# Kernel tuning notes

Hardware: AMD Instinct MI355X
Metric: run time of the kernel (lower is better)

## Reference

```python
import jax, jax.numpy as jnp
import numpy as np

B, C, H, W = 4, 512, 48, 48
BN_EPS = 1e-5


def setup_inputs() -> dict:
    key = jax.random.key(0)
    ks = jax.random.split(key, 12)
    s = 1.0 / np.sqrt(C)  # conv2d default init scale for 1x1 kernels
    return {
        "x": jax.random.normal(ks[0], (B, C, H, W), dtype=jnp.float32),
        "from_depth_estimation": jax.random.normal(ks[1], (B, C, H, W), dtype=jnp.float32),
        "w_rgb": jax.random.uniform(ks[2], (C, C), jnp.float32, -s, s),
        "b_rgb": jax.random.uniform(ks[3], (C,), jnp.float32, -s, s),
        "w_lhs": jax.random.uniform(ks[4], (C, C), jnp.float32, -s, s),
        "b_lhs": jax.random.uniform(ks[5], (C,), jnp.float32, -s, s),
        "w_rhs": jax.random.uniform(ks[6], (C, C), jnp.float32, -s, s),
        "b_rhs": jax.random.uniform(ks[7], (C,), jnp.float32, -s, s),
        "w_dec": jax.random.uniform(ks[8], (C, C), jnp.float32, -s, s),
        "b_dec": jax.random.uniform(ks[9], (C,), jnp.float32, -s, s),
        "gamma": jnp.ones((C,), jnp.float32),
        "beta": jnp.zeros((C,), jnp.float32),
    }


def _to_tokens(t):
    # (B,C,H,W) -> (B*H*W, C)
    return t.transpose(0, 2, 3, 1).reshape(-1, t.shape[1])


def reference(x, from_depth_estimation, w_rgb, b_rgb, w_lhs, b_lhs, w_rhs, b_rhs,
              w_dec, b_dec, gamma, beta):
    # 1x1 convs == per-token linear layers; weight layout (out, in)
    xt = _to_tokens(x) @ w_rgb.T + b_rgb          # (N, C)
    dt = _to_tokens(from_depth_estimation)
    lhs = dt @ w_lhs.T + b_lhs                     # (N, C)
    rhs = dt @ w_rhs.T + b_rhs                     # (N, C)

    # global, unscaled attention over all B*H*W tokens (batch dims mixed)
    logits = lhs @ rhs.T                           # (N, N)
    weight = jax.nn.softmax(logits, axis=1)
    enhanced = weight @ xt                         # (N, C)

    enhanced = enhanced.reshape(B, H, W, C).transpose(0, 3, 1, 2)  # (B,C,H,W)

    # decoder: 1x1 conv -> BatchNorm2d (batch stats, training mode) -> ReLU
    y = jnp.einsum('bchw,oc->bohw', enhanced, w_dec) + b_dec[None, :, None, None]
    mean = y.mean(axis=(0, 2, 3), keepdims=True)
    var = y.var(axis=(0, 2, 3), keepdims=True)     # biased variance (torch BN fwd)
    y = (y - mean) * jax.lax.rsqrt(var + BN_EPS)
    y = y * gamma[None, :, None, None] + beta[None, :, None, None]
    return jax.nn.relu(y)
```

## Files before the change

kernel.cpp:

```cpp
#include <hip/hip_runtime.h>
#include <math.h>

#define Bd 4
#define Cd 512
#define Hd 48
#define Wd 48
#define HWd (Hd * Wd)
#define Nd (Bd * HWd)
#define BN_EPS 1e-5f

#define QBLK 32
#define KBLK 128
#define NKS 4
#define KSLEN (Nd / NKS)
#define AITERS (KSLEN / KBLK)

typedef _Float16 half8 __attribute__((ext_vector_type(8)));
typedef _Float16 h4 __attribute__((ext_vector_type(4)));
typedef float f32x16 __attribute__((ext_vector_type(16)));

__device__ inline void gload_lds16(const void* g, void* l) {
    __builtin_amdgcn_global_load_lds((const __attribute__((address_space(1))) void*)g,
                                     (__attribute__((address_space(3))) void*)l, 16, 0, 0);
}

__device__ inline size_t wp_idx(int o, int c) {
    return (((size_t)(o >> 5) * 32 + (c >> 4)) * 64 + ((o & 31) + 32 * ((c >> 3) & 1))) * 8 + (c & 7);
}
__device__ inline size_t qp_idx(int q, int c) {
    return (((size_t)(q >> 5) * 64 + (c >> 3)) * 32 + (q & 31)) * 8 + (c & 7);
}
__device__ inline size_t kp_idx(int n, int o) {
    return ((((size_t)(n >> 7) * 4 + ((n >> 5) & 3)) * 32 + (o >> 4)) * 64
            + ((n & 31) + 32 * ((o >> 3) & 1))) * 8 + (o & 7);
}
__device__ inline size_t vp_idx(int n, int o) {
    return ((((size_t)(n >> 7) * 16 + (o >> 5)) * 8 + ((n >> 4) & 7)) * 64
            + ((o & 31) + 32 * ((n >> 3) & 1))) * 8 + (n & 7);
}

__global__ __launch_bounds__(256) void wpack_k(const float* __restrict__ w0,
                                               const float* __restrict__ w1,
                                               const float* __restrict__ w2,
                                               const float* __restrict__ w3,
                                               _Float16* __restrict__ p0,
                                               _Float16* __restrict__ p1,
                                               _Float16* __restrict__ p2,
                                               _Float16* __restrict__ p3) {
    const float* w; _Float16* p;
    switch (blockIdx.y) {
        case 0: w = w0; p = p0; break;
        case 1: w = w1; p = p1; break;
        case 2: w = w2; p = p2; break;
        default: w = w3; p = p3; break;
    }
    int idx = blockIdx.x * 256 + threadIdx.x;
    int o = idx >> 6;
    int cc = (idx & 63) * 8;
    float4 a = *(const float4*)(w + (size_t)o * 512 + cc);
    float4 b = *(const float4*)(w + (size_t)o * 512 + cc + 4);
    half8 v = {(_Float16)a.x, (_Float16)a.y, (_Float16)a.z, (_Float16)a.w,
               (_Float16)b.x, (_Float16)b.y, (_Float16)b.z, (_Float16)b.w};
    *(half8*)(p + wp_idx(o, cc)) = v;
}

template<int INM, int OUTM>
__global__ __launch_bounds__(256, 2) void linproj_k(const void* __restrict__ in,
                                                    const _Float16* __restrict__ Wp,
                                                    const float* __restrict__ bias,
                                                    void* __restrict__ outp) {
    constexpr bool SWAP = (OUTM == 2);
    __shared__ _Float16 Xs[16384];

    const int tid = threadIdx.x;
    const int wave = tid >> 6;
    const int lane = tid & 63;
    const int l31 = lane & 31;
    const int hi32 = lane >> 5;
    const int n0 = blockIdx.x * 32;
    const int by = blockIdx.y;
    const int b = n0 / HWd;
    const int hw0 = n0 % HWd;

    {
        const int t = tid & 31;
        const int c0 = tid >> 5;
        #pragma unroll 8
        for (int k = 0; k < 64; ++k) {
            int c = c0 + 8 * k;
            float val;
            if (INM == 0)
                val = ((const float*)in)[(size_t)(b * Cd + c) * HWd + hw0 + t];
            else
                val = (float)((const _Float16*)in)[(size_t)c * Nd + n0 + t];
            if (!SWAP)
                Xs[(c >> 3) * 256 + t * 8 + (c & 7)] = (_Float16)val;
            else
                Xs[(c >> 4) * 512 + (t + 32 * ((c >> 3) & 1)) * 8 + (c & 7)] = (_Float16)val;
        }
    }
    __syncthreads();

    #pragma unroll
    for (int ot = 0; ot < 2; ++ot) {
        const int otb = by * 256 + ot * 128 + wave * 32;

        half8 wa[32];
        const _Float16* wpb = Wp + ((size_t)(otb >> 5) * 32) * 512;
        #pragma unroll
        for (int f = 0; f < 32; ++f)
            wa[f] = *(const half8*)(wpb + (size_t)f * 512 + lane * 8);

        f32x16 acc;
        #pragma unroll
        for (int r = 0; r < 16; ++r) acc[r] = 0.f;

        __builtin_amdgcn_s_setprio(1);
        #pragma unroll
        for (int f = 0; f < 32; ++f) {
            if (!SWAP) {
                half8 xb = *(const half8*)(Xs + (2 * f + hi32) * 256 + l31 * 8);
                acc = __builtin_amdgcn_mfma_f32_32x32x16_f16(wa[f], xb, acc, 0, 0, 0);
            } else {
                half8 xa = *(const half8*)(Xs + f * 512 + lane * 8);
                acc = __builtin_amdgcn_mfma_f32_32x32x16_f16(xa, wa[f], acc, 0, 0, 0);
            }
        }
        __builtin_amdgcn_s_setprio(0);

        if (OUTM == 0) {
            _Float16* Qp = (_Float16*)outp;
            #pragma unroll
            for (int q8 = 0; q8 < 4; ++q8) {
                int o = otb + 8 * q8 + 4 * hi32;
                float4 bv = *(const float4*)(bias + o);
                h4 v = {(_Float16)(acc[4 * q8 + 0] + bv.x), (_Float16)(acc[4 * q8 + 1] + bv.y),
                        (_Float16)(acc[4 * q8 + 2] + bv.z), (_Float16)(acc[4 * q8 + 3] + bv.w)};
                *(h4*)(Qp + qp_idx(n0 + l31, o)) = v;
            }
        } else if (OUTM == 1) {
            _Float16* Kp = (_Float16*)outp;
            #pragma unroll
            for (int q8 = 0; q8 < 4; ++q8) {
                int o = otb + 8 * q8 + 4 * hi32;
                float4 bv = *(const float4*)(bias + o);
                h4 v = {(_Float16)(acc[4 * q8 + 0] + bv.x), (_Float16)(acc[4 * q8 + 1] + bv.y),
                        (_Float16)(acc[4 * q8 + 2] + bv.z), (_Float16)(acc[4 * q8 + 3] + bv.w)};
                *(h4*)(Kp + kp_idx(n0 + l31, o)) = v;
            }
        } else if (OUTM == 2) {
            _Float16* Vp = (_Float16*)outp;
            int o = otb + l31;
            float bc = bias[o];
            #pragma unroll
            for (int q8 = 0; q8 < 4; ++q8) {
                int n = n0 + 8 * q8 + 4 * hi32;
                h4 v = {(_Float16)(acc[4 * q8 + 0] + bc), (_Float16)(acc[4 * q8 + 1] + bc),
                        (_Float16)(acc[4 * q8 + 2] + bc), (_Float16)(acc[4 * q8 + 3] + bc)};
                *(h4*)(Vp + vp_idx(n, o)) = v;
            }
        } else {
            float* of = (float*)outp;
            #pragma unroll
            for (int r = 0; r < 16; ++r) {
                int o = otb + (r & 3) + 8 * (r >> 2) + 4 * hi32;
                of[(size_t)(b * Cd + o) * HWd + hw0 + l31] = acc[r] + bias[o];
            }
        }
    }
}

__global__ __launch_bounds__(256, 2) void attn_v5_k(
    const _Float16* __restrict__ Qp,
    const _Float16* __restrict__ Kp,
    const _Float16* __restrict__ Vp,
    _Float16* __restrict__ partH,
    float* __restrict__ marr,
    float* __restrict__ larr) {
    __shared__ _Float16 Qs[64 * 256];
    __shared__ _Float16 Pl[2][16 * 256];
    __shared__ float tm_s[4][32], ls_s[4][32];

    const int tid = threadIdx.x;
    const int wave = tid >> 6;
    const int lane = tid & 63;
    const int l31 = lane & 31;
    const int hi32 = lane >> 5;
    const int nqb = Nd / QBLK;
    const int qb = blockIdx.x % nqb;
    const int ks = blockIdx.x / nqb;
    const int q0 = qb * QBLK;
    const int kbt0 = ks * AITERS;

    {
        const _Float16* Qt = Qp + (size_t)(q0 >> 5) * 16384;
        #pragma unroll
        for (int j = 0; j < 8; ++j) {
            int instr = wave * 8 + j;
            gload_lds16(Qt + (size_t)instr * 512 + lane * 8, (char*)Qs + instr * 1024);
        }
    }
    __syncthreads();

    f32x16 o_acc[4];
    #pragma unroll
    for (int c = 0; c < 4; ++c)
        #pragma unroll
        for (int r = 0; r < 16; ++r) o_acc[c][r] = 0.f;
    float m = -INFINITY, l = 0.f;

    for (int it = 0; it < AITERS; ++it) {
        const _Float16* kp = Kp + ((size_t)(kbt0 + it) * 4 + wave) * 32 * 512;
        half8 ka[32];
        #pragma unroll
        for (int f = 0; f < 32; ++f)
            ka[f] = *(const half8*)(kp + (size_t)f * 512 + lane * 8);

        f32x16 s;
        #pragma unroll
        for (int r = 0; r < 16; ++r) s[r] = 0.f;
        __builtin_amdgcn_s_setprio(1);
        #pragma unroll
        for (int f = 0; f < 32; ++f) {
            half8 qb8 = *(const half8*)(Qs + (2 * f + hi32) * 256 + l31 * 8);
            s = __builtin_amdgcn_mfma_f32_32x32x16_f16(ka[f], qb8, s, 0, 0, 0);
        }
        __builtin_amdgcn_s_setprio(0);

        float tmax = s[0];
        #pragma unroll
        for (int r = 1; r < 16; ++r) tmax = fmaxf(tmax, s[r]);
        tmax = fmaxf(tmax, __shfl_xor(tmax, 32));
        if (lane < 32) tm_s[wave][lane] = tmax;
        __syncthreads();

        float mn = fmaxf(fmaxf(fmaxf(tm_s[0][l31], tm_s[1][l31]),
                               fmaxf(tm_s[2][l31], tm_s[3][l31])), m);
        float corr = __expf(m - mn);

        float p[16];
        float psum = 0.f;
        #pragma unroll
        for (int r = 0; r < 16; ++r) { p[r] = __expf(s[r] - mn); psum += p[r]; }
        {
            char* pbuf = (char*)Pl[it & 1];
            #pragma unroll
            for (int g = 0; g < 8; ++g) {
                int r0 = 2 * g;
                int krow = (r0 & 3) + 8 * (r0 >> 2) + 4 * hi32 + 32 * wave;
                _Float16 two[2] = {(_Float16)p[r0], (_Float16)p[r0 + 1]};
                *(unsigned*)(pbuf + ((krow >> 3) * 512 + l31 * 16 + (krow & 7) * 2)) =
                    *(unsigned*)two;
            }
        }
        psum += __shfl_xor(psum, 32);
        if (lane < 32) ls_s[wave][lane] = psum;
        __syncthreads();

        l = l * corr + (ls_s[0][l31] + ls_s[1][l31]) + (ls_s[2][l31] + ls_s[3][l31]);
        m = mn;

        const _Float16* vpb = Vp + (size_t)(kbt0 + it) * 16 * 8 * 512
                            + (size_t)wave * 4 * 8 * 512;
        half8 va[32];
        #pragma unroll
        for (int kf = 0; kf < 8; ++kf)
            #pragma unroll
            for (int cht = 0; cht < 4; ++cht)
                va[kf * 4 + cht] =
                    *(const half8*)(vpb + ((size_t)cht * 8 + kf) * 512 + lane * 8);

        #pragma unroll
        for (int c = 0; c < 4; ++c)
            #pragma unroll
            for (int r = 0; r < 16; ++r) o_acc[c][r] *= corr;

        const _Float16* pbuf = Pl[it & 1];
        __builtin_amdgcn_s_setprio(1);
        #pragma unroll
        for (int kf = 0; kf < 8; ++kf) {
            half8 pfrag = *(const half8*)(pbuf + (2 * kf + hi32) * 256 + l31 * 8);
            #pragma unroll
            for (int cht = 0; cht < 4; ++cht)
                o_acc[cht] = __builtin_amdgcn_mfma_f32_32x32x16_f16(
                    va[kf * 4 + cht], pfrag, o_acc[cht], 0, 0, 0);
        }
        __builtin_amdgcn_s_setprio(0);
    }

    float linv = 1.f / l;
    #pragma unroll
    for (int cht = 0; cht < 4; ++cht)
        #pragma unroll
        for (int r = 0; r < 16; ++r) {
            int row = (r & 3) + 8 * (r >> 2) + 4 * hi32;
            partH[((size_t)ks * Cd + wave * 128 + cht * 32 + row) * Nd + q0 + l31] =
                (_Float16)(o_acc[cht][r] * linv);
        }
    if (wave == 0 && lane < 32) {
        marr[(size_t)ks * Nd + q0 + lane] = m;
        larr[(size_t)ks * Nd + q0 + lane] = l;
    }
}

__global__ __launch_bounds__(256) void merge4_k(_Float16* __restrict__ partH,
                                                const float* __restrict__ marr,
                                                const float* __restrict__ larr) {
    size_t idx = (size_t)blockIdx.x * 256 + threadIdx.x;
    if (idx >= (size_t)Cd * Nd) return;
    int q = (int)(idx % Nd);
    float mv[NKS], wv[NKS];
    float mm = -INFINITY;
    #pragma unroll
    for (int s = 0; s < NKS; ++s) { mv[s] = marr[(size_t)s * Nd + q]; mm = fmaxf(mm, mv[s]); }
    float L = 0.f;
    #pragma unroll
    for (int s = 0; s < NKS; ++s) {
        wv[s] = larr[(size_t)s * Nd + q] * __expf(mv[s] - mm);
        L += wv[s];
    }
    float val = 0.f;
    #pragma unroll
    for (int s = 0; s < NKS; ++s)
        val += wv[s] * (float)partH[(size_t)s * Cd * Nd + idx];
    partH[idx] = (_Float16)(val / L);
}

__global__ __launch_bounds__(256) void bnstats_k(const float* __restrict__ y,
                                                 const float* __restrict__ gamma,
                                                 const float* __restrict__ beta,
                                                 float* __restrict__ stats) {
    const int c = blockIdx.x;
    const int tid = threadIdx.x;
    double s = 0.0, sq = 0.0;
    for (int b = 0; b < Bd; ++b) {
        const float* p = y + (size_t)(b * Cd + c) * HWd;
        for (int i = tid; i < HWd; i += 256) {
            double v = (double)p[i];
            s += v;
            sq += v * v;
        }
    }
    #pragma unroll
    for (int off = 32; off; off >>= 1) {
        s  += __shfl_xor(s, off, 64);
        sq += __shfl_xor(sq, off, 64);
    }
    __shared__ double ss[4], sqs[4];
    int wid = tid >> 6;
    if ((tid & 63) == 0) { ss[wid] = s; sqs[wid] = sq; }
    __syncthreads();
    if (tid == 0) {
        double S = ss[0] + ss[1] + ss[2] + ss[3];
        double Q = sqs[0] + sqs[1] + sqs[2] + sqs[3];
        double mean = S / (double)Nd;
        double var = Q / (double)Nd - mean * mean;
        float inv = (float)(1.0 / sqrt(var + (double)BN_EPS));
        float sc = gamma[c] * inv;
        stats[c] = sc;
        stats[Cd + c] = beta[c] - (float)mean * sc;
    }
}

__global__ __launch_bounds__(256) void bnapply_k(float* __restrict__ y,
                                                 const float* __restrict__ stats) {
    int idx = blockIdx.x * 256 + threadIdx.x;
    if (idx >= Bd * Cd * HWd) return;
    int c = (idx / HWd) % Cd;
    float v = fmaf(y[idx], stats[c], stats[Cd + c]);
    y[idx] = fmaxf(v, 0.f);
}

extern "C" void kernel_launch(void* const* d_in, const int* in_sizes, int n_in,
                              void* d_out, int out_size, void* d_ws, size_t ws_size,
                              hipStream_t stream) {
    const float* x     = (const float*)d_in[0];
    const float* depth = (const float*)d_in[1];
    const float* w_rgb = (const float*)d_in[2];
    const float* b_rgb = (const float*)d_in[3];
    const float* w_lhs = (const float*)d_in[4];
    const float* b_lhs = (const float*)d_in[5];
    const float* w_rhs = (const float*)d_in[6];
    const float* b_rhs = (const float*)d_in[7];
    const float* w_dec = (const float*)d_in[8];
    const float* b_dec = (const float*)d_in[9];
    const float* gamma = (const float*)d_in[10];
    const float* beta  = (const float*)d_in[11];
    float* out = (float*)d_out;

    char* wsb = (char*)d_ws;
    const size_t NC = (size_t)Nd * Cd;
    _Float16* Qp    = (_Float16*)wsb;
    _Float16* Kp    = (_Float16*)(wsb + NC * 2);
    _Float16* Vp    = (_Float16*)(wsb + NC * 4);
    _Float16* partH = (_Float16*)(wsb + NC * 6);
    float* marr  = (float*)(wsb + NC * 6 + NKS * NC * 2);
    float* larr  = marr + (size_t)NKS * Nd;
    float* stats = larr + (size_t)NKS * Nd;
    _Float16* wpLhs = (_Float16*)(stats + 2 * Cd);
    _Float16* wpRhs = wpLhs + (size_t)Cd * Cd;
    _Float16* wpRgb = wpRhs + (size_t)Cd * Cd;
    _Float16* wpDec = wpRgb + (size_t)Cd * Cd;

    wpack_k<<<dim3(128, 4), 256, 0, stream>>>(w_lhs, w_rhs, w_rgb, w_dec,
                                              wpLhs, wpRhs, wpRgb, wpDec);

    dim3 gLin(Nd / 32, 2);
    linproj_k<0, 0><<<gLin, 256, 0, stream>>>(depth, wpLhs, b_lhs, Qp);
    linproj_k<0, 1><<<gLin, 256, 0, stream>>>(depth, wpRhs, b_rhs, Kp);
    linproj_k<0, 2><<<gLin, 256, 0, stream>>>(x, wpRgb, b_rgb, Vp);

    attn_v5_k<<<(Nd / QBLK) * NKS, 256, 0, stream>>>(Qp, Kp, Vp, partH, marr, larr);

    merge4_k<<<(int)((NC + 255) / 256), 256, 0, stream>>>(partH, marr, larr);

    linproj_k<3, 3><<<gLin, 256, 0, stream>>>(partH, wpDec, b_dec, out);

    bnstats_k<<<Cd, 256, 0, stream>>>(out, gamma, beta, stats);
    bnapply_k<<<(Bd * Cd * HWd + 255) / 256, 256, 0, stream>>>(out, stats);
}
```

Measured before the change: 384.7 us.

## Double query block per attention workgroup to halve K/V global reloads

New measurement: 371.1 us. 1.04x faster.

```diff
diff --git a/kernel.cpp b/kernel.cpp
--- a/kernel.cpp
+++ b/kernel.cpp
@@ -9,7 +9,7 @@
 #define Nd (Bd * HWd)
 #define BN_EPS 1e-5f
 
-#define QBLK 32
+#define QBLK 64
 #define KBLK 128
 #define NKS 4
 #define KSLEN (Nd / NKS)
@@ -170,22 +170,24 @@
     }
 }
 
-__global__ __launch_bounds__(256, 2) void attn_v5_k(
+__global__ __launch_bounds__(512, 2) void attn_v6_k(
     const _Float16* __restrict__ Qp,
     const _Float16* __restrict__ Kp,
     const _Float16* __restrict__ Vp,
     _Float16* __restrict__ partH,
     float* __restrict__ marr,
     float* __restrict__ larr) {
-    __shared__ _Float16 Qs[64 * 256];
-    __shared__ _Float16 Pl[2][16 * 256];
-    __shared__ float tm_s[4][32], ls_s[4][32];
+    __shared__ _Float16 Qs[2 * 16384];
+    __shared__ _Float16 Pl[8192];
+    __shared__ float tm_s[4][64], ls_s[4][64];
 
     const int tid = threadIdx.x;
     const int wave = tid >> 6;
     const int lane = tid & 63;
     const int l31 = lane & 31;
     const int hi32 = lane >> 5;
+    const int kt = wave & 3;
+    const int qg = wave >> 2;
     const int nqb = Nd / QBLK;
     const int qb = blockIdx.x % nqb;
     const int ks = blockIdx.x / nqb;
@@ -195,22 +197,23 @@
     {
         const _Float16* Qt = Qp + (size_t)(q0 >> 5) * 16384;
         #pragma unroll
-        for (int j = 0; j < 8; ++j) {
-            int instr = wave * 8 + j;
-            gload_lds16(Qt + (size_t)instr * 512 + lane * 8, (char*)Qs + instr * 1024);
-        }
+        for (int j = 0; j < 8; ++j)
+            gload_lds16(Qt + (size_t)j * 4096 + tid * 8,
+                        (char*)Qs + j * 8192 + wave * 1024);
     }
     __syncthreads();
 
-    f32x16 o_acc[4];
-    #pragma unroll
-    for (int c = 0; c < 4; ++c)
-        #pragma unroll
-        for (int r = 0; r < 16; ++r) o_acc[c][r] = 0.f;
-    float m = -INFINITY, l = 0.f;
+    f32x16 o_acc[2][2];
+    #pragma unroll
+    for (int c = 0; c < 2; ++c)
+        #pragma unroll
+        for (int q = 0; q < 2; ++q)
+            #pragma unroll
+            for (int r = 0; r < 16; ++r) o_acc[c][q][r] = 0.f;
+    float m0 = -INFINITY, m1 = -INFINITY, l0 = 0.f, l1 = 0.f;
 
     for (int it = 0; it < AITERS; ++it) {
-        const _Float16* kp = Kp + ((size_t)(kbt0 + it) * 4 + wave) * 32 * 512;
+        const _Float16* kp = Kp + ((size_t)(kbt0 + it) * 4 + kt) * 32 * 512;
         half8 ka[32];
         #pragma unroll
         for (int f = 0; f < 32; ++f)
@@ -219,10 +222,11 @@
         f32x16 s;
         #pragma unroll
         for (int r = 0; r < 16; ++r) s[r] = 0.f;
+        const _Float16* qsb = Qs + qg * 16384;
         __builtin_amdgcn_s_setprio(1);
         #pragma unroll
         for (int f = 0; f < 32; ++f) {
-            half8 qb8 = *(const half8*)(Qs + (2 * f + hi32) * 256 + l31 * 8);
+            half8 qb8 = *(const half8*)(qsb + (2 * f + hi32) * 256 + l31 * 8);
             s = __builtin_amdgcn_mfma_f32_32x32x16_f16(ka[f], qb8, s, 0, 0, 0);
         }
         __builtin_amdgcn_s_setprio(0);
@@ -231,75 +235,87 @@
         #pragma unroll
         for (int r = 1; r < 16; ++r) tmax = fmaxf(tmax, s[r]);
         tmax = fmaxf(tmax, __shfl_xor(tmax, 32));
-        if (lane < 32) tm_s[wave][lane] = tmax;
+        if (lane < 32) tm_s[kt][qg * 32 + lane] = tmax;
         __syncthreads();
 
-        float mn = fmaxf(fmaxf(fmaxf(tm_s[0][l31], tm_s[1][l31]),
-                               fmaxf(tm_s[2][l31], tm_s[3][l31])), m);
-        float corr = __expf(m - mn);
+        float mn0 = fmaxf(fmaxf(fmaxf(tm_s[0][l31], tm_s[1][l31]),
+                                fmaxf(tm_s[2][l31], tm_s[3][l31])), m0);
+        float mn1 = fmaxf(fmaxf(fmaxf(tm_s[0][32 + l31], tm_s[1][32 + l31]),
+                                fmaxf(tm_s[2][32 + l31], tm_s[3][32 + l31])), m1);
+        float corr0 = __expf(m0 - mn0);
+        float corr1 = __expf(m1 - mn1);
+        float mn_own = qg ? mn1 : mn0;
 
         float p[16];
         float psum = 0.f;
         #pragma unroll
-        for (int r = 0; r < 16; ++r) { p[r] = __expf(s[r] - mn); psum += p[r]; }
-        {
-            char* pbuf = (char*)Pl[it & 1];
-            #pragma unroll
-            for (int g = 0; g < 8; ++g) {
-                int r0 = 2 * g;
-                int krow = (r0 & 3) + 8 * (r0 >> 2) + 4 * hi32 + 32 * wave;
-                _Float16 two[2] = {(_Float16)p[r0], (_Float16)p[r0 + 1]};
-                *(unsigned*)(pbuf + ((krow >> 3) * 512 + l31 * 16 + (krow & 7) * 2)) =
-                    *(unsigned*)two;
-            }
+        for (int r = 0; r < 16; ++r) { p[r] = __expf(s[r] - mn_own); psum += p[r]; }
+        #pragma unroll
+        for (int g = 0; g < 4; ++g) {
+            h4 v = {(_Float16)p[4 * g + 0], (_Float16)p[4 * g + 1],
+                    (_Float16)p[4 * g + 2], (_Float16)p[4 * g + 3]};
+            *(h4*)(Pl + (qg * 8 + kt * 2 + (g >> 1)) * 512 + (g & 1) * 256
+                      + l31 * 8 + 4 * hi32) = v;
         }
         psum += __shfl_xor(psum, 32);
-        if (lane < 32) ls_s[wave][lane] = psum;
+        if (lane < 32) ls_s[kt][qg * 32 + lane] = psum;
         __syncthreads();
 
-        l = l * corr + (ls_s[0][l31] + ls_s[1][l31]) + (ls_s[2][l31] + ls_s[3][l31]);
-        m = mn;
-
-        const _Float16* vpb = Vp + (size_t)(kbt0 + it) * 16 * 8 * 512
-                            + (size_t)wave * 4 * 8 * 512;
-        half8 va[32];
-        #pragma unroll
-        for (int kf = 0; kf < 8; ++kf)
-            #pragma unroll
-            for (int cht = 0; cht < 4; ++cht)
-                va[kf * 4 + cht] =
-                    *(const half8*)(vpb + ((size_t)cht * 8 + kf) * 512 + lane * 8);
-
-        #pragma unroll
-        for (int c = 0; c < 4; ++c)
-            #pragma unroll
-            for (int r = 0; r < 16; ++r) o_acc[c][r] *= corr;
-
-        const _Float16* pbuf = Pl[it & 1];
+        l0 = l0 * corr0 + (ls_s[0][l31] + ls_s[1][l31]) + (ls_s[2][l31] + ls_s[3][l31]);
+        l1 = l1 * corr1 + (ls_s[0][32 + l31] + ls_s[1][32 + l31])
+                        + (ls_s[2][32 + l31] + ls_s[3][32 + l31]);
+        m0 = mn0; m1 = mn1;
+
+        half8 va[16];
+        #pragma unroll
+        for (int cht = 0; cht < 2; ++cht)
+            #pragma unroll
+            for (int kc = 0; kc < 8; ++kc)
+                va[cht * 8 + kc] = *(const half8*)(
+                    Vp + (((size_t)(kbt0 + it) * 16 + wave * 2 + cht) * 8 + kc) * 512
+                       + lane * 8);
+
+        #pragma unroll
+        for (int cht = 0; cht < 2; ++cht)
+            #pragma unroll
+            for (int r = 0; r < 16; ++r) {
+                o_acc[cht][0][r] *= corr0;
+                o_acc[cht][1][r] *= corr1;
+            }
+
         __builtin_amdgcn_s_setprio(1);
         #pragma unroll
-        for (int kf = 0; kf < 8; ++kf) {
-            half8 pfrag = *(const half8*)(pbuf + (2 * kf + hi32) * 256 + l31 * 8);
-            #pragma unroll
-            for (int cht = 0; cht < 4; ++cht)
-                o_acc[cht] = __builtin_amdgcn_mfma_f32_32x32x16_f16(
-                    va[kf * 4 + cht], pfrag, o_acc[cht], 0, 0, 0);
-        }
+        for (int qt = 0; qt < 2; ++qt)
+            #pragma unroll
+            for (int kc = 0; kc < 8; ++kc) {
+                half8 pfrag = *(const half8*)(Pl + (qt * 8 + kc) * 512
+                                                 + hi32 * 256 + l31 * 8);
+                #pragma unroll
+                for (int cht = 0; cht < 2; ++cht)
+                    o_acc[cht][qt] = __builtin_amdgcn_mfma_f32_32x32x16_f16(
+                        va[cht * 8 + kc], pfrag, o_acc[cht][qt], 0, 0, 0);
+            }
         __builtin_amdgcn_s_setprio(0);
     }
 
-    float linv = 1.f / l;
-    #pragma unroll
-    for (int cht = 0; cht < 4; ++cht)
-        #pragma unroll
-        for (int r = 0; r < 16; ++r) {
-            int row = (r & 3) + 8 * (r >> 2) + 4 * hi32;
-            partH[((size_t)ks * Cd + wave * 128 + cht * 32 + row) * Nd + q0 + l31] =
-                (_Float16)(o_acc[cht][r] * linv);
-        }
+    float li0 = 1.f / l0, li1 = 1.f / l1;
+    #pragma unroll
+    for (int cht = 0; cht < 2; ++cht)
+        #pragma unroll
+        for (int qt = 0; qt < 2; ++qt)
+            #pragma unroll
+            for (int r = 0; r < 16; ++r) {
+                int row = (r & 3) + 8 * (r >> 2) + 4 * hi32;
+                int ch = wave * 64 + cht * 32 + row;
+                int q = q0 + qt * 32 + l31;
+                partH[((size_t)ks * Cd + ch) * Nd + q] =
+                    (_Float16)(o_acc[cht][qt][r] * (qt ? li1 : li0));
+            }
     if (wave == 0 && lane < 32) {
-        marr[(size_t)ks * Nd + q0 + lane] = m;
-        larr[(size_t)ks * Nd + q0 + lane] = l;
+        marr[(size_t)ks * Nd + q0 + lane] = m0;
+        larr[(size_t)ks * Nd + q0 + lane] = l0;
+        marr[(size_t)ks * Nd + q0 + 32 + lane] = m1;
+        larr[(size_t)ks * Nd + q0 + 32 + lane] = l1;
     }
 }
 
@@ -410,7 +426,7 @@
     linproj_k<0, 1><<<gLin, 256, 0, stream>>>(depth, wpRhs, b_rhs, Kp);
     linproj_k<0, 2><<<gLin, 256, 0, stream>>>(x, wpRgb, b_rgb, Vp);
 
-    attn_v5_k<<<(Nd / QBLK) * NKS, 256, 0, stream>>>(Qp, Kp, Vp, partH, marr, larr);
+    attn_v6_k<<<(Nd / QBLK) * NKS, 512, 0, stream>>>(Qp, Kp, Vp, partH, marr, larr);
 
     merge4_k<<<(int)((NC + 255) / 256), 256, 0, stream>>>(partH, marr, larr);
 
```
